# Optimization experiments

Measured on AMD Instinct MI355X. Metric: run time of the kernel, lower is better.

The kernel has to match this reference:

```python
import jax, jax.numpy as jnp
import numpy as np

B, L, LI = 128, 64, 64
DATA, HID, WID = 16, 128, 256


def _sorted_times(key, b, n, t0, t1):
    u = jnp.sort(jax.random.uniform(key, (b, n)), axis=1)
    u = (u - u[:, :1]) / (u[:, -1:] - u[:, :1])
    return t0 + u * (t1 - t0)


def setup_inputs() -> dict:
    key = jax.random.key(0)
    ks = jax.random.split(key, 20)
    def lin(k, out, inp):
        return (jax.random.normal(k, (out, inp)) / np.sqrt(inp)).astype(jnp.float32)
    return {
        "ts": _sorted_times(ks[0], B, L, 0.0, 10.0),
        "ts_interp": _sorted_times(ks[1], B, LI, 0.0, 10.0),
        "obs_interp": jax.random.normal(ks[2], (B, LI, DATA), dtype=jnp.float32),
        "tmax": (5.0 + 4.0 * jax.random.uniform(ks[3], (B,))).astype(jnp.float32),
        "i_win": lin(ks[4], WID, DATA),
        "i_bin": jnp.zeros((WID,), jnp.float32),
        "i_wmid": jnp.stack([lin(ks[5], WID, WID), lin(ks[6], WID, WID)]),
        "i_bmid": jnp.zeros((2, WID), jnp.float32),
        "i_wout": lin(ks[7], HID, WID),
        "i_bout": jnp.zeros((HID,), jnp.float32),
        "v_win": lin(ks[8], WID, HID),
        "v_bin": jnp.zeros((WID,), jnp.float32),
        "v_wmid": jnp.stack([lin(ks[9], WID, WID), lin(ks[10], WID, WID)]),
        "v_bmid": jnp.zeros((2, WID), jnp.float32),
        "v_wout": lin(ks[11], HID * DATA, WID),
        "v_bout": jnp.zeros((HID * DATA,), jnp.float32),
    }


def _mlp(y, w_in, b_in, w_mid, b_mid, w_out, b_out, final_act):
    # eqx.nn.MLP with softplus activation, depth=3: in->W, W->W, W->W, W->out
    h = jax.nn.softplus(y @ w_in.T + b_in)
    for i in range(w_mid.shape[0]):
        h = jax.nn.softplus(h @ w_mid[i].T + b_mid[i])
    return final_act(h @ w_out.T + b_out)


def _seg_idx(knots, t):
    return jnp.clip(jnp.searchsorted(knots, t, side='right') - 1, 0, knots.shape[0] - 2)


def _ctrl_eval(knots, vals, t):  # LinearInterpolation.evaluate, per sample
    j = _seg_idx(knots, t)
    frac = (t - knots[j]) / (knots[j + 1] - knots[j])
    return vals[j] + frac * (vals[j + 1] - vals[j])


def _ctrl_deriv(knots, vals, t):  # LinearInterpolation.derivative (piecewise const)
    j = _seg_idx(knots, t)
    return (vals[j + 1] - vals[j]) / (knots[j + 1] - knots[j])


def reference(ts, ts_interp, obs_interp, tmax,
              i_win, i_bin, i_wmid, i_bmid, i_wout, i_bout,
              v_win, v_bin, v_wmid, v_bmid, v_wout, v_bout):
    ctrl_eval = jax.vmap(_ctrl_eval)
    ctrl_deriv = jax.vmap(_ctrl_deriv)

    x0 = ctrl_eval(ts_interp, obs_interp, ts[:, 0])              # [B, DATA]
    y0 = _mlp(x0, i_win, i_bin, i_wmid, i_bmid, i_wout, i_bout, lambda z: z)  # [B, HID]

    def f(t, y):  # ControlTerm(vf, control).to_ode(): vf(y) @ dX/dt
        a = _mlp(y, v_win, v_bin, v_wmid, v_bmid, v_wout, v_bout, jnp.tanh)
        a = a.reshape(y.shape[0], HID, DATA)
        dx = ctrl_deriv(ts_interp, obs_interp, t)                # [B, DATA]
        return jnp.einsum('bhd,bd->bh', a, dx)

    def step(y, tt):  # one RK4 step per save interval (fixed-step reference)
        t0, t1 = tt
        dt = t1 - t0
        h = dt[:, None]
        k1 = f(t0, y)
        k2 = f(t0 + 0.5 * dt, y + 0.5 * h * k1)
        k3 = f(t0 + 0.5 * dt, y + 0.5 * h * k2)
        k4 = f(t1, y + h * k3)
        yn = y + (h / 6.0) * (k1 + 2.0 * k2 + 2.0 * k3 + k4)
        return yn, yn

    t_pairs = (ts[:, :-1].T, ts[:, 1:].T)   # scan over L-1 intervals, each [B]
    _, ys = jax.lax.scan(step, y0, t_pairs)  # [L-1, B, HID]
    ys = jnp.concatenate([y0[None], ys], axis=0)      # [L, B, HID]
    ys = jnp.transpose(ys, (1, 0, 2))                  # [B, L, HID]
    mask = ts <= tmax[:, None]
    return jnp.where(mask[:, :, None], ys, jnp.float32(-99.0))
```

## Files before the change

### kernel.cpp

```cpp
#include <hip/hip_runtime.h>
#include <stdint.h>


#define NB   256
#define NTHR 512

#define SC_OFF   0u
#define WV_OFF   11264u
#define WM1_OFF  76800u
#define WL4_OFF  207872u
#define WM0_OFF  1256448u
#define EX_OFF   1387520u

typedef unsigned long long u64t;

static __device__ __forceinline__ u64t ld_coh8(const u64t* p) {
  return __hip_atomic_load(p, __ATOMIC_RELAXED, __HIP_MEMORY_SCOPE_AGENT);
}
static __device__ __forceinline__ void st_coh8(u64t* p, u64t v) {
  __hip_atomic_store(p, v, __ATOMIC_RELAXED, __HIP_MEMORY_SCOPE_AGENT);
}
static __device__ __forceinline__ u64t pack_tf(float f, uint32_t tag) {
  union { float f; uint32_t u; } c; c.f = f;
  return ((u64t)tag << 32) | c.u;
}
static __device__ __forceinline__ float low_f(u64t v) {
  union { uint32_t u; float f; } c; c.u = (uint32_t)v;
  return c.f;
}

static __device__ __forceinline__ float qmac2(uint32_t q, float h0, float h1, float acc) {
  acc = fmaf((float)(short)(q & 0xffffu), h0, acc);
  return fmaf((float)(short)(q >> 16), h1, acc);
}

static __device__ __forceinline__ float sp_fast(float x) {
  return fmaxf(x, 0.f) + __logf(1.f + __expf(-fabsf(x)));
}
static __device__ __forceinline__ float sp(float x) {
  return fmaxf(x, 0.f) + log1pf(expf(-fabsf(x)));
}
static __device__ __forceinline__ float tanh_fast(float x) {
  float ax = fabsf(x);
  float e = __expf(ax + ax);
  float t = 1.f - 2.f * __builtin_amdgcn_rcpf(e + 1.f);
  return __builtin_copysignf(t, x);
}

static __device__ __forceinline__ void lbar() {
  asm volatile("s_waitcnt lgkmcnt(0)\n\ts_barrier" ::: "memory");
}

static __device__ __forceinline__ int seg_idx(const float* kn, float t) {
  int lo = 0, hi = 64;
  while (lo < hi) { int mid = (lo + hi) >> 1; if (kn[mid] <= t) lo = mid + 1; else hi = mid; }
  int jj = lo - 1;
  return jj < 0 ? 0 : (jj > 62 ? 62 : jj);
}

__global__ void prep_kernel(const float* __restrict__ v_win,
                            const float* __restrict__ v_wmid,
                            const float* __restrict__ v_wout,
                            unsigned char* __restrict__ wsb) {
  float* scales = (float*)(wsb + SC_OFF);
  short* wv  = (short*)(wsb + WV_OFF);
  short* wm1 = (short*)(wsb + WM1_OFF);
  short* wl4 = (short*)(wsb + WL4_OFF);
  short* wm0 = (short*)(wsb + WM0_OFF);
  const int r = blockIdx.x, lane = threadIdx.x;
  const float* src;
  int n;
  if (r < 256)       { src = v_win  + (size_t)r * 128;                 n = 128; }
  else if (r < 512)  { src = v_wmid + 65536 + (size_t)(r - 256) * 256; n = 256; }
  else if (r < 2560) { src = v_wout + (size_t)(r - 512) * 256;         n = 256; }
  else               { src = v_wmid + (size_t)(r - 2560) * 256;        n = 256; }
  float m = 0.f;
  for (int i = lane; i < n; i += 64) m = fmaxf(m, fabsf(src[i]));
#pragma unroll
  for (int off = 32; off; off >>= 1) m = fmaxf(m, __shfl_xor(m, off));
  const float inv = (m > 0.f) ? 32767.f / m : 0.f;
  if (lane == 0) scales[r] = (m > 0.f) ? m / 32767.f : 1.f;
  for (int i = lane; i < n; i += 64) {
    short q = (short)rintf(src[i] * inv);
    if (r < 256) {
      int hf = i >> 6, c = (i & 63) >> 3, e = i & 7;
      wv[c * 4096 + (2 * r + hf) * 8 + e] = q;
    } else if (r < 512) {
      int row = r - 256, hf = i >> 7, c = (i & 127) >> 3, e = i & 7;
      wm1[c * 4096 + (2 * row + hf) * 8 + e] = q;
    } else if (r < 2560) {
      int row = r - 512;
      int h = row >> 4, d = row & 15;
      int s = h >> 6, h_loc = h & 63, dgrp = d >> 1, rs = d & 1;
      int t = h_loc * 8 + dgrp;
      int cc = i >> 3, e = i & 7;
      wl4[s * 262144 + ((rs * 32 + cc) * 512 + t) * 8 + e] = q;
    } else {
      int row = r - 2560;
      wm0[(size_t)row * 256 + i] = q;
    }
  }
}

__global__ void __launch_bounds__(NTHR)
ncde_kernel(const float* __restrict__ ts, const float* __restrict__ tsi,
            const float* __restrict__ obs, const float* __restrict__ tmax,
            const float* __restrict__ i_win, const float* __restrict__ i_bin,
            const float* __restrict__ i_wmid, const float* __restrict__ i_bmid,
            const float* __restrict__ i_wout, const float* __restrict__ i_bout,
            const float* __restrict__ v_wmid, const float* __restrict__ v_bin,
            const float* __restrict__ v_bmid, const float* __restrict__ v_bout,
            unsigned char* __restrict__ wsb, float* __restrict__ out) {
  __shared__ __align__(16) uint32_t s_m0[256][132];
  __shared__ __align__(16) float s_yin[128];
  __shared__ __align__(16) float s_h1[256];
  __shared__ __align__(16) float s_h2[256];
  __shared__ __align__(16) float s_h3[256];
  __shared__ __align__(16) float s_ts[64];
  __shared__ __align__(16) float s_kn[64];
  __shared__ __align__(16) float s_dxt[127][16];
  __shared__ float s_y[128];
  __shared__ float s_k[128];
  __shared__ float s_ka[128];
  __shared__ float s_x0[16];
  __shared__ unsigned char s_sj[128];

  const int t = threadIdx.x;
  const int bid = blockIdx.x;
  const int b = bid & 127;
  const int s = bid >> 7;
  const int o = t >> 1, half = t & 1;

  const float* scales = (const float*)(wsb + SC_OFF);
  const uint4* wvp  = ((const uint4*)(wsb + WV_OFF)) + t;
  const uint4* wm1p = ((const uint4*)(wsb + WM1_OFF)) + t;
  const uint4* wl4p = ((const uint4*)(wsb + WL4_OFF)) + s * 32768 + t;
  u64t* exb    = ((u64t*)(wsb + EX_OFF)) + (size_t)b * 256;
  u64t* ex_own = exb + s * 128;
  u64t* expart = exb + (1 - s) * 128;

  if (t < 64) { s_ts[t] = ts[b * 64 + t]; s_kn[t] = tsi[b * 64 + t]; }
  const float tm = tmax[b];
  const float bl1 = v_bin[o];
  const float bm0 = v_bmid[o];
  const float bm1 = v_bmid[256 + o];
  const float sc_wv = scales[o];
  const float sc_m1 = scales[256 + o];
  const float sc_m0 = scales[2560 + o];
  const int r0 = ((s << 6) + (t >> 3)) * 16 + 2 * (t & 7);
  const float2 scl4 = *(const float2*)(scales + 512 + r0);
  const float2 vb2  = *(const float2*)(v_bout + r0);
  __syncthreads();

  {
    const uint32_t* wm0u = (const uint32_t*)(wsb + WM0_OFF);
    for (int idx = t; idx < 32768; idx += NTHR) {
      int row = idx >> 7, k = idx & 127;
      s_m0[row][k ^ (((row >> 3) & 3) << 2)] = wm0u[idx];
    }
  }
  if (t < 127) {
    int li = t >> 1;
    float te = (t & 1) ? fmaf(0.5f, s_ts[li + 1] - s_ts[li], s_ts[li]) : s_ts[li];
    s_sj[t] = (unsigned char)seg_idx(s_kn, te);
  }
  __syncthreads();

  for (int idx = t; idx < 127 * 16; idx += NTHR) {
    int ti = idx >> 4, d = idx & 15;
    int sj = s_sj[ti];
    const float* ob = obs + ((size_t)b * 64 + sj) * 16 + d;
    s_dxt[ti][d] = (ob[16] - ob[0]) / (s_kn[sj + 1] - s_kn[sj]);
  }

  if (t < 16) {
    float t0 = s_ts[0];
    int sj = seg_idx(s_kn, t0);
    float k0 = s_kn[sj], k1 = s_kn[sj + 1];
    float fr = (t0 - k0) / (k1 - k0);
    const float* ob = obs + ((size_t)b * 64 + sj) * 16 + t;
    s_x0[t] = fmaf(fr, ob[16] - ob[0], ob[0]);
  }
  __syncthreads();
  if (t < 256) {
    float acc = i_bin[t];
    const float* wr = i_win + (size_t)t * 16;
#pragma unroll
    for (int i = 0; i < 16; ++i) acc = fmaf(wr[i], s_x0[i], acc);
    s_h1[t] = sp(acc);
  }
  __syncthreads();
  {
    float acc = 0.f;
    const float4* wq = (const float4*)(i_wmid + (size_t)o * 256 + half * 128);
    const float4* hp = (const float4*)(s_h1 + half * 128);
#pragma unroll
    for (int i = 0; i < 32; ++i) {
      float4 w = wq[i]; float4 hh = hp[i];
      acc = fmaf(w.x, hh.x, acc); acc = fmaf(w.y, hh.y, acc);
      acc = fmaf(w.z, hh.z, acc); acc = fmaf(w.w, hh.w, acc);
    }
    acc += __shfl_xor(acc, 1);
    if (!half) s_h2[o] = sp(acc + i_bmid[o]);
  }
  __syncthreads();
  {
    float acc = 0.f;
    const float4* wq = (const float4*)(i_wmid + 65536 + (size_t)o * 256 + half * 128);
    const float4* hp = (const float4*)(s_h2 + half * 128);
#pragma unroll
    for (int i = 0; i < 32; ++i) {
      float4 w = wq[i]; float4 hh = hp[i];
      acc = fmaf(w.x, hh.x, acc); acc = fmaf(w.y, hh.y, acc);
      acc = fmaf(w.z, hh.z, acc); acc = fmaf(w.w, hh.w, acc);
    }
    acc += __shfl_xor(acc, 1);
    if (!half) s_h3[o] = sp(acc + i_bmid[256 + o]);
  }
  __syncthreads();
  {
    float acc = 0.f;
    const float4* wq = (const float4*)(i_wout + (size_t)(t >> 2) * 256 + (t & 3) * 64);
    const float4* hp = (const float4*)(s_h3 + (t & 3) * 64);
#pragma unroll
    for (int i = 0; i < 16; ++i) {
      float4 w = wq[i]; float4 hh = hp[i];
      acc = fmaf(w.x, hh.x, acc); acc = fmaf(w.y, hh.y, acc);
      acc = fmaf(w.z, hh.z, acc); acc = fmaf(w.w, hh.w, acc);
    }
    acc += __shfl_xor(acc, 1);
    acc += __shfl_xor(acc, 2);
    if ((t & 3) == 0) {
      int h = t >> 2;
      float y0 = acc + i_bout[h];
      s_y[h] = y0;
      if (s == 0)
        out[(size_t)b * 8192 + h] = (s_ts[0] <= tm) ? y0 : -99.f;
    }
  }
  __syncthreads();

#pragma unroll 1
  for (int l = 0; l < 63; ++l) {
    const float dt = s_ts[l + 1] - s_ts[l];
    const float dtp = (l > 0) ? (s_ts[l] - s_ts[l - 1]) : 0.f;
#pragma unroll 1
    for (int e = 0; e < 4; ++e) {
      const int ti = 2 * l + ((e == 0) ? 0 : ((e == 3) ? 2 : 1));
      auto upd = [&](int h, float kv) {
        if (e == 0) {
          float ka = s_ka[h] + kv;
          float yn = fmaf(dtp * (1.f / 6.f), ka, s_y[h]);
          s_y[h] = yn;
          s_yin[h] = yn;
          if (s == 0)
            out[(size_t)b * 8192 + (size_t)l * 128 + h] =
                (s_ts[l] <= tm) ? yn : -99.f;
        } else {
          float ka = (e == 1) ? kv : fmaf(2.f, kv, s_ka[h]);
          s_ka[h] = ka;
          float ce = (e == 3) ? 1.f : 0.5f;
          s_yin[h] = fmaf(ce * dt, kv, s_y[h]);
        }
      };
      if (l == 0 && e == 0) {
        if (t < 128) s_yin[t] = s_y[t];
      } else {
        const uint32_t tg = (uint32_t)(l * 4 + e);
        if (t < 64) {
          u64t* pw = expart + ((tg & 1) << 6) + t;
          u64t v = ld_coh8(pw);
          uint32_t n = 0;
          while ((uint32_t)(v >> 32) != tg) {
            if (n > 8) __builtin_amdgcn_s_sleep(8);
            else       __builtin_amdgcn_s_sleep(1);
            if (++n > (1u << 14)) break;
            v = ld_coh8(pw);
          }
          upd((1 - s) * 64 + t, low_f(v));
        } else if (t < 128) {
          int ho = s * 64 + (t - 64);
          upd(ho, s_k[ho]);
        }
      }
      lbar();
      {
        float acc = 0.f;
#pragma unroll
        for (int c = 0; c < 8; ++c) {
          uint4 w = wvp[c * 512];
          float4 ya = *(const float4*)(s_yin + half * 64 + 8 * c);
          float4 yb = *(const float4*)(s_yin + half * 64 + 8 * c + 4);
          acc = qmac2(w.x, ya.x, ya.y, acc);
          acc = qmac2(w.y, ya.z, ya.w, acc);
          acc = qmac2(w.z, yb.x, yb.y, acc);
          acc = qmac2(w.w, yb.z, yb.w, acc);
        }
        acc += __shfl_xor(acc, 1);
        if (!half) s_h1[o] = sp_fast(acc * sc_wv + bl1);
      }
      lbar();
      {
        float acc = 0.f;
        const int swz = ((o >> 3) & 3) << 2;
        const uint32_t* wr = &s_m0[o][0];
#pragma unroll
        for (int k = 0; k < 16; ++k) {
          uint4 w = *(const uint4*)(wr + (((half * 64 + 4 * k)) ^ swz));
          float4 ha = *(const float4*)(s_h1 + half * 128 + 8 * k);
          float4 hb = *(const float4*)(s_h1 + half * 128 + 8 * k + 4);
          acc = qmac2(w.x, ha.x, ha.y, acc);
          acc = qmac2(w.y, ha.z, ha.w, acc);
          acc = qmac2(w.z, hb.x, hb.y, acc);
          acc = qmac2(w.w, hb.z, hb.w, acc);
        }
        acc += __shfl_xor(acc, 1);
        if (!half) s_h2[o] = sp_fast(acc * sc_m0 + bm0);
      }
      lbar();
      {
        float acc = 0.f;
#pragma unroll 4
        for (int c = 0; c < 16; ++c) {
          uint4 w = wm1p[c * 512];
          float4 ha = *(const float4*)(s_h2 + half * 128 + 8 * c);
          float4 hb = *(const float4*)(s_h2 + half * 128 + 8 * c + 4);
          acc = qmac2(w.x, ha.x, ha.y, acc);
          acc = qmac2(w.y, ha.z, ha.w, acc);
          acc = qmac2(w.z, hb.x, hb.y, acc);
          acc = qmac2(w.w, hb.z, hb.w, acc);
        }
        acc += __shfl_xor(acc, 1);
        if (!half) s_h3[o] = sp_fast(acc * sc_m1 + bm1);
      }
      lbar();
      {
        float z0 = 0.f, z1 = 0.f;
#pragma unroll 4
        for (int cc = 0; cc < 32; ++cc) {
          float4 ha = *(const float4*)(s_h3 + 8 * cc);
          float4 hb = *(const float4*)(s_h3 + 8 * cc + 4);
          uint4 w0 = wl4p[cc * 512];
          uint4 w1 = wl4p[(32 + cc) * 512];
          z0 = qmac2(w0.x, ha.x, ha.y, z0); z0 = qmac2(w0.y, ha.z, ha.w, z0);
          z0 = qmac2(w0.z, hb.x, hb.y, z0); z0 = qmac2(w0.w, hb.z, hb.w, z0);
          z1 = qmac2(w1.x, ha.x, ha.y, z1); z1 = qmac2(w1.y, ha.z, ha.w, z1);
          z1 = qmac2(w1.z, hb.x, hb.y, z1); z1 = qmac2(w1.w, hb.z, hb.w, z1);
        }
        const int d0 = 2 * (t & 7);
        float kv;
        kv = tanh_fast(fmaf(z0, scl4.x, vb2.x)) * s_dxt[ti][d0];
        kv = fmaf(tanh_fast(fmaf(z1, scl4.y, vb2.y)), s_dxt[ti][d0 + 1], kv);
        kv += __shfl_xor(kv, 1);
        kv += __shfl_xor(kv, 2);
        kv += __shfl_xor(kv, 4);
        if ((t & 7) == 0) {
          const uint32_t T = (uint32_t)(l * 4 + e + 1);
          int h_loc = t >> 3;
          s_k[(s << 6) + h_loc] = kv;
          st_coh8(ex_own + ((T & 1) << 6) + h_loc, pack_tf(kv, T));
        }
      }
      lbar();
    }
  }

  if (s == 0) {
    const float dtp = s_ts[63] - s_ts[62];
    if (t < 64) {
      u64t* pw = expart + t;
      u64t v = ld_coh8(pw);
      uint32_t n = 0;
      while ((uint32_t)(v >> 32) != 252u) {
        if (n > 8) __builtin_amdgcn_s_sleep(8);
        else       __builtin_amdgcn_s_sleep(1);
        if (++n > (1u << 14)) break;
        v = ld_coh8(pw);
      }
      int h = 64 + t;
      float ka = s_ka[h] + low_f(v);
      float yn = fmaf(dtp * (1.f / 6.f), ka, s_y[h]);
      out[(size_t)b * 8192 + 63 * 128 + h] = (s_ts[63] <= tm) ? yn : -99.f;
    } else if (t < 128) {
      int h = t - 64;
      float ka = s_ka[h] + s_k[h];
      float yn = fmaf(dtp * (1.f / 6.f), ka, s_y[h]);
      out[(size_t)b * 8192 + 63 * 128 + h] = (s_ts[63] <= tm) ? yn : -99.f;
    }
  }
}

extern "C" void kernel_launch(void* const* d_in, const int* in_sizes, int n_in,
                              void* d_out, int out_size, void* d_ws, size_t ws_size,
                              hipStream_t stream) {
  const float* ts     = (const float*)d_in[0];
  const float* tsi    = (const float*)d_in[1];
  const float* obs    = (const float*)d_in[2];
  const float* tmaxp  = (const float*)d_in[3];
  const float* i_win  = (const float*)d_in[4];
  const float* i_bin  = (const float*)d_in[5];
  const float* i_wmid = (const float*)d_in[6];
  const float* i_bmid = (const float*)d_in[7];
  const float* i_wout = (const float*)d_in[8];
  const float* i_bout = (const float*)d_in[9];
  const float* v_win  = (const float*)d_in[10];
  const float* v_bin  = (const float*)d_in[11];
  const float* v_wmid = (const float*)d_in[12];
  const float* v_bmid = (const float*)d_in[13];
  const float* v_wout = (const float*)d_in[14];
  const float* v_bout = (const float*)d_in[15];

  unsigned char* wsb = (unsigned char*)d_ws;

  size_t exbytes = 262144;
  if (EX_OFF + exbytes > ws_size) exbytes = (ws_size > EX_OFF) ? ws_size - EX_OFF : 0;
  (void)hipMemsetAsync(wsb + EX_OFF, 0, exbytes, stream);

  prep_kernel<<<dim3(2816), dim3(64), 0, stream>>>(v_win, v_wmid, v_wout, wsb);
  ncde_kernel<<<dim3(NB), dim3(NTHR), 0, stream>>>(
      ts, tsi, obs, tmaxp,
      i_win, i_bin, i_wmid, i_bmid, i_wout, i_bout,
      v_wmid, v_bin, v_bmid, v_bout,
      wsb, (float*)d_out);
}
```

Before: 2.552 ms.

## Double threads per block to 1024 and re-split MLP dot products four ways

Raises the block size from 512 to 1024 threads and changes every per-step matvec to use four threads per output row instead of two, with an extra shuffle reduction. The quantized weight layouts for the vector-field layers are repacked to match the new per-thread slicing. The final output layer now gives one (hidden, data) output per thread instead of two. The aim is to shorten the serial per-thread dot-product chain in the latency-bound RK4 loop, at the cost of more shuffles, more barrier participants and fewer registers per thread.

```diff
diff --git a/kernel.cpp b/kernel.cpp
--- a/kernel.cpp
+++ b/kernel.cpp
@@ -3,7 +3,7 @@
 
 
 #define NB   256
-#define NTHR 512
+#define NTHR 1024
 
 #define SC_OFF   0u
 #define WV_OFF   11264u
@@ -81,28 +81,27 @@
   const float inv = (m > 0.f) ? 32767.f / m : 0.f;
   if (lane == 0) scales[r] = (m > 0.f) ? m / 32767.f : 1.f;
   for (int i = lane; i < n; i += 64) {
-    short q = (short)rintf(src[i] * inv);
+    short qv = (short)rintf(src[i] * inv);
     if (r < 256) {
-      int hf = i >> 6, c = (i & 63) >> 3, e = i & 7;
-      wv[c * 4096 + (2 * r + hf) * 8 + e] = q;
+      int qd = i >> 5, c = (i & 31) >> 3, e = i & 7;
+      wv[(c * 1024 + 4 * r + qd) * 8 + e] = qv;
     } else if (r < 512) {
-      int row = r - 256, hf = i >> 7, c = (i & 127) >> 3, e = i & 7;
-      wm1[c * 4096 + (2 * row + hf) * 8 + e] = q;
+      int row = r - 256;
+      int qd = i >> 6, c = (i & 63) >> 3, e = i & 7;
+      wm1[(c * 1024 + 4 * row + qd) * 8 + e] = qv;
     } else if (r < 2560) {
       int row = r - 512;
-      int h = row >> 4, d = row & 15;
-      int s = h >> 6, h_loc = h & 63, dgrp = d >> 1, rs = d & 1;
-      int t = h_loc * 8 + dgrp;
-      int cc = i >> 3, e = i & 7;
-      wl4[s * 262144 + ((rs * 32 + cc) * 512 + t) * 8 + e] = q;
+      int s = row >> 10, row_s = row & 1023;
+      int c = i >> 3, e = i & 7;
+      wl4[s * 262144 + (c * 1024 + row_s) * 8 + e] = qv;
     } else {
       int row = r - 2560;
-      wm0[(size_t)row * 256 + i] = q;
-    }
-  }
-}
-
-__global__ void __launch_bounds__(NTHR)
+      wm0[(size_t)row * 256 + i] = qv;
+    }
+  }
+}
+
+__global__ void __launch_bounds__(NTHR, 4)
 ncde_kernel(const float* __restrict__ ts, const float* __restrict__ tsi,
             const float* __restrict__ obs, const float* __restrict__ tmax,
             const float* __restrict__ i_win, const float* __restrict__ i_bin,
@@ -129,7 +128,8 @@
   const int bid = blockIdx.x;
   const int b = bid & 127;
   const int s = bid >> 7;
-  const int o = t >> 1, half = t & 1;
+  const int o = t >> 2, q = t & 3;
+  const int dL = t & 15, hl = t >> 4;
 
   const float* scales = (const float*)(wsb + SC_OFF);
   const uint4* wvp  = ((const uint4*)(wsb + WV_OFF)) + t;
@@ -147,9 +147,8 @@
   const float sc_wv = scales[o];
   const float sc_m1 = scales[256 + o];
   const float sc_m0 = scales[2560 + o];
-  const int r0 = ((s << 6) + (t >> 3)) * 16 + 2 * (t & 7);
-  const float2 scl4 = *(const float2*)(scales + 512 + r0);
-  const float2 vb2  = *(const float2*)(v_bout + r0);
+  const float scl4f = scales[512 + s * 1024 + t];
+  const float vbf   = v_bout[s * 1024 + t];
   __syncthreads();
 
   {
@@ -190,10 +189,11 @@
     s_h1[t] = sp(acc);
   }
   __syncthreads();
-  {
+  if (t < 512) {
+    int oi = t >> 1, hf = t & 1;
     float acc = 0.f;
-    const float4* wq = (const float4*)(i_wmid + (size_t)o * 256 + half * 128);
-    const float4* hp = (const float4*)(s_h1 + half * 128);
+    const float4* wq = (const float4*)(i_wmid + (size_t)oi * 256 + hf * 128);
+    const float4* hp = (const float4*)(s_h1 + hf * 128);
 #pragma unroll
     for (int i = 0; i < 32; ++i) {
       float4 w = wq[i]; float4 hh = hp[i];
@@ -201,13 +201,14 @@
       acc = fmaf(w.z, hh.z, acc); acc = fmaf(w.w, hh.w, acc);
     }
     acc += __shfl_xor(acc, 1);
-    if (!half) s_h2[o] = sp(acc + i_bmid[o]);
-  }
-  __syncthreads();
-  {
+    if (!hf) s_h2[oi] = sp(acc + i_bmid[oi]);
+  }
+  __syncthreads();
+  if (t < 512) {
+    int oi = t >> 1, hf = t & 1;
     float acc = 0.f;
-    const float4* wq = (const float4*)(i_wmid + 65536 + (size_t)o * 256 + half * 128);
-    const float4* hp = (const float4*)(s_h2 + half * 128);
+    const float4* wq = (const float4*)(i_wmid + 65536 + (size_t)oi * 256 + hf * 128);
+    const float4* hp = (const float4*)(s_h2 + hf * 128);
 #pragma unroll
     for (int i = 0; i < 32; ++i) {
       float4 w = wq[i]; float4 hh = hp[i];
@@ -215,10 +216,10 @@
       acc = fmaf(w.z, hh.z, acc); acc = fmaf(w.w, hh.w, acc);
     }
     acc += __shfl_xor(acc, 1);
-    if (!half) s_h3[o] = sp(acc + i_bmid[256 + o]);
-  }
-  __syncthreads();
-  {
+    if (!hf) s_h3[oi] = sp(acc + i_bmid[256 + oi]);
+  }
+  __syncthreads();
+  if (t < 512) {
     float acc = 0.f;
     const float4* wq = (const float4*)(i_wout + (size_t)(t >> 2) * 256 + (t & 3) * 64);
     const float4* hp = (const float4*)(s_h3 + (t & 3) * 64);
@@ -287,17 +288,18 @@
       {
         float acc = 0.f;
 #pragma unroll
-        for (int c = 0; c < 8; ++c) {
-          uint4 w = wvp[c * 512];
-          float4 ya = *(const float4*)(s_yin + half * 64 + 8 * c);
-          float4 yb = *(const float4*)(s_yin + half * 64 + 8 * c + 4);
+        for (int c = 0; c < 4; ++c) {
+          uint4 w = wvp[c * 1024];
+          float4 ya = *(const float4*)(s_yin + q * 32 + 8 * c);
+          float4 yb = *(const float4*)(s_yin + q * 32 + 8 * c + 4);
           acc = qmac2(w.x, ya.x, ya.y, acc);
           acc = qmac2(w.y, ya.z, ya.w, acc);
           acc = qmac2(w.z, yb.x, yb.y, acc);
           acc = qmac2(w.w, yb.z, yb.w, acc);
         }
         acc += __shfl_xor(acc, 1);
-        if (!half) s_h1[o] = sp_fast(acc * sc_wv + bl1);
+        acc += __shfl_xor(acc, 2);
+        if (q == 0) s_h1[o] = sp_fast(acc * sc_wv + bl1);
       }
       lbar();
       {
@@ -305,60 +307,62 @@
         const int swz = ((o >> 3) & 3) << 2;
         const uint32_t* wr = &s_m0[o][0];
 #pragma unroll
-        for (int k = 0; k < 16; ++k) {
-          uint4 w = *(const uint4*)(wr + (((half * 64 + 4 * k)) ^ swz));
-          float4 ha = *(const float4*)(s_h1 + half * 128 + 8 * k);
-          float4 hb = *(const float4*)(s_h1 + half * 128 + 8 * k + 4);
+        for (int k = 0; k < 8; ++k) {
+          uint4 w = *(const uint4*)(wr + ((q * 32 + 4 * k) ^ swz));
+          float4 ha = *(const float4*)(s_h1 + q * 64 + 8 * k);
+          float4 hb = *(const float4*)(s_h1 + q * 64 + 8 * k + 4);
           acc = qmac2(w.x, ha.x, ha.y, acc);
           acc = qmac2(w.y, ha.z, ha.w, acc);
           acc = qmac2(w.z, hb.x, hb.y, acc);
           acc = qmac2(w.w, hb.z, hb.w, acc);
         }
         acc += __shfl_xor(acc, 1);
-        if (!half) s_h2[o] = sp_fast(acc * sc_m0 + bm0);
+        acc += __shfl_xor(acc, 2);
+        if (q == 0) s_h2[o] = sp_fast(acc * sc_m0 + bm0);
       }
       lbar();
       {
         float acc = 0.f;
-#pragma unroll 4
-        for (int c = 0; c < 16; ++c) {
-          uint4 w = wm1p[c * 512];
-          float4 ha = *(const float4*)(s_h2 + half * 128 + 8 * c);
-          float4 hb = *(const float4*)(s_h2 + half * 128 + 8 * c + 4);
+#pragma unroll
+        for (int c = 0; c < 8; ++c) {
+          uint4 w = wm1p[c * 1024];
+          float4 ha = *(const float4*)(s_h2 + q * 64 + 8 * c);
+          float4 hb = *(const float4*)(s_h2 + q * 64 + 8 * c + 4);
           acc = qmac2(w.x, ha.x, ha.y, acc);
           acc = qmac2(w.y, ha.z, ha.w, acc);
           acc = qmac2(w.z, hb.x, hb.y, acc);
           acc = qmac2(w.w, hb.z, hb.w, acc);
         }
         acc += __shfl_xor(acc, 1);
-        if (!half) s_h3[o] = sp_fast(acc * sc_m1 + bm1);
+        acc += __shfl_xor(acc, 2);
+        if (q == 0) s_h3[o] = sp_fast(acc * sc_m1 + bm1);
       }
       lbar();
       {
-        float z0 = 0.f, z1 = 0.f;
+        float za = 0.f, zb = 0.f;
 #pragma unroll 4
-        for (int cc = 0; cc < 32; ++cc) {
-          float4 ha = *(const float4*)(s_h3 + 8 * cc);
-          float4 hb = *(const float4*)(s_h3 + 8 * cc + 4);
-          uint4 w0 = wl4p[cc * 512];
-          uint4 w1 = wl4p[(32 + cc) * 512];
-          z0 = qmac2(w0.x, ha.x, ha.y, z0); z0 = qmac2(w0.y, ha.z, ha.w, z0);
-          z0 = qmac2(w0.z, hb.x, hb.y, z0); z0 = qmac2(w0.w, hb.z, hb.w, z0);
-          z1 = qmac2(w1.x, ha.x, ha.y, z1); z1 = qmac2(w1.y, ha.z, ha.w, z1);
-          z1 = qmac2(w1.z, hb.x, hb.y, z1); z1 = qmac2(w1.w, hb.z, hb.w, z1);
-        }
-        const int d0 = 2 * (t & 7);
-        float kv;
-        kv = tanh_fast(fmaf(z0, scl4.x, vb2.x)) * s_dxt[ti][d0];
-        kv = fmaf(tanh_fast(fmaf(z1, scl4.y, vb2.y)), s_dxt[ti][d0 + 1], kv);
+        for (int cc = 0; cc < 32; cc += 2) {
+          float4 ha0 = *(const float4*)(s_h3 + 8 * cc);
+          float4 hb0 = *(const float4*)(s_h3 + 8 * cc + 4);
+          uint4 w0 = wl4p[cc * 1024];
+          float4 ha1 = *(const float4*)(s_h3 + 8 * cc + 8);
+          float4 hb1 = *(const float4*)(s_h3 + 8 * cc + 12);
+          uint4 w1 = wl4p[(cc + 1) * 1024];
+          za = qmac2(w0.x, ha0.x, ha0.y, za); za = qmac2(w0.y, ha0.z, ha0.w, za);
+          za = qmac2(w0.z, hb0.x, hb0.y, za); za = qmac2(w0.w, hb0.z, hb0.w, za);
+          zb = qmac2(w1.x, ha1.x, ha1.y, zb); zb = qmac2(w1.y, ha1.z, ha1.w, zb);
+          zb = qmac2(w1.z, hb1.x, hb1.y, zb); zb = qmac2(w1.w, hb1.z, hb1.w, zb);
+        }
+        float z = za + zb;
+        float kv = tanh_fast(fmaf(z, scl4f, vbf)) * s_dxt[ti][dL];
         kv += __shfl_xor(kv, 1);
         kv += __shfl_xor(kv, 2);
         kv += __shfl_xor(kv, 4);
-        if ((t & 7) == 0) {
+        kv += __shfl_xor(kv, 8);
+        if (dL == 0) {
           const uint32_t T = (uint32_t)(l * 4 + e + 1);
-          int h_loc = t >> 3;
-          s_k[(s << 6) + h_loc] = kv;
-          st_coh8(ex_own + ((T & 1) << 6) + h_loc, pack_tf(kv, T));
+          s_k[(s << 6) + hl] = kv;
+          st_coh8(ex_own + ((T & 1) << 6) + hl, pack_tf(kv, T));
         }
       }
       lbar();
```

Result: slower. 3.289 ms (+28.9%).
